# Kernel tuning notes

Measured on AMD Instinct MI355X. Metric: run time of the kernel, lower is better.

Reference implementation:

```python
import jax, jax.numpy as jnp
import numpy as np

KLD_SCALE = 10.0


def setup_inputs() -> dict:
    key = jax.random.key(0)
    k1, k2 = jax.random.split(key)
    B, C, H, W = 16, 64, 64, 64
    K = 1024
    inputs = jax.random.normal(k1, (B, C, H, W), dtype=jnp.float32)
    codebook = jax.random.normal(k2, (K, C), dtype=jnp.float32) * (1.0 / K)
    beta = jnp.float32(0.25)
    return {"inputs": inputs, "codebook": codebook, "beta": beta}


def reference(inputs, codebook, beta):
    # inputs: [B, C, H, W], codebook: [K, D] with D == C
    sg = jax.lax.stop_gradient
    x = jnp.transpose(inputs, (0, 2, 3, 1))          # [B, H, W, D]
    D = x.shape[-1]
    flat = x.reshape(-1, D)                           # [N, D]
    d = (jnp.sum(flat * flat, axis=1, keepdims=True)
         + jnp.sum(codebook * codebook, axis=1)
         - 2.0 * flat @ codebook.T)                   # [N, K]
    idx = jnp.argmin(d, axis=1)                       # [N]
    q = codebook[idx].reshape(x.shape)                # gather == one_hot @ codebook
    # training (non-EMA) loss: (beta*||q - sg(x)||^2 + ||sg(q) - x||^2) * kld_scale
    loss = beta * jnp.mean((q - sg(x)) ** 2)
    loss = (loss + jnp.mean((sg(q) - x) ** 2)) * KLD_SCALE
    # straight-through estimator
    q_st = x + sg(q - x)
    # perplexity from code usage histogram (== mean of one-hot rows)
    K = codebook.shape[0]
    counts = jnp.zeros((K,), dtype=flat.dtype).at[idx].add(1.0)
    e_mean = counts / flat.shape[0]
    perplexity = jnp.exp(-jnp.sum(e_mean * jnp.log(e_mean + 1e-10)))
    quantized = jnp.transpose(q_st, (0, 3, 1, 2))     # [B, C, H, W]
    return loss, quantized, perplexity
```

## Files before the change

### kernel.cpp

```cpp
#include <hip/hip_runtime.h>
#include <cfloat>

typedef __bf16 bf16x8 __attribute__((ext_vector_type(8)));
typedef float f32x16 __attribute__((ext_vector_type(16)));

namespace {
constexpr int kHW = 4096;
constexpr int kC = 64;
constexpr float kInvN = 1.0f / 65536.0f;


__global__ __launch_bounds__(256) void prep_kernel(
    const float* __restrict__ cb, uint4* __restrict__ frags,
    unsigned int* __restrict__ hist, float* __restrict__ lossacc) {
  const int c = blockIdx.x;
  const int t = threadIdx.x;
  const int lane = t & 63, wv = t >> 6;
  const int lo = lane & 31, hi = lane >> 5;
  const int code = c * 32 + lo;
  const int ks = wv;

  const float* row = cb + code * kC + ks * 16 + hi * 8;
  float4 v0 = *reinterpret_cast<const float4*>(row);
  float4 v1 = *reinterpret_cast<const float4*>(row + 4);
  float vv[8] = {v0.x, v0.y, v0.z, v0.w, v1.x, v1.y, v1.z, v1.w};
  bf16x8 fh, fl;
  #pragma unroll
  for (int e = 0; e < 8; ++e) {
    float v = -2.0f * vv[e];
    __bf16 h = (__bf16)v;
    fh[e] = h;
    fl[e] = (__bf16)(v - (float)h);
  }
  frags[(c * 9 + ks) * 64 + lane] = *reinterpret_cast<uint4*>(&fh);
  frags[(c * 9 + 4 + ks) * 64 + lane] = *reinterpret_cast<uint4*>(&fl);

  if (wv == 0) {
    bf16x8 fb;
    #pragma unroll
    for (int e = 0; e < 8; ++e) fb[e] = (__bf16)0.0f;
    if (hi == 0) {
      float s = 0.0f;
      #pragma unroll
      for (int d = 0; d < kC; d += 4) {
        float4 v = *reinterpret_cast<const float4*>(cb + code * kC + d);
        s = fmaf(v.x, v.x, fmaf(v.y, v.y, fmaf(v.z, v.z, fmaf(v.w, v.w, s))));
      }
      __bf16 h = (__bf16)s;
      fb[0] = h;
      fb[1] = (__bf16)(s - (float)h);
    }
    frags[(c * 9 + 8) * 64 + lane] = *reinterpret_cast<uint4*>(&fb);
  }
  if (t < 32) hist[c * 32 + t] = 0u;
  if (c == 0 && t == 0) lossacc[0] = 0.0f;
}

__global__ __launch_bounds__(256) void vq_kernel(
    const float* __restrict__ in, const bf16x8* __restrict__ frags,
    const float* __restrict__ cb, unsigned int* __restrict__ hist,
    float* __restrict__ lossacc, float* __restrict__ qout) {
  __shared__ float sVal[4][32];
  __shared__ int sIdxW[4][32];
  __shared__ int sIdx[64];
  const int t = threadIdx.x;
  const int lane = t & 63, wv = t >> 6;
  const int lo = lane & 31, hi = lane >> 5;
  const int sg2 = wv & 1, kh = wv >> 1;
  const int site = blockIdx.x * 64 + sg2 * 32 + lo;
  const int b = site >> 12, hw = site & 4095;
  const float* xp = in + b * (kC * kHW) + hw;

  bf16x8 Bh[4], Bl[4];
  #pragma unroll
  for (int ks = 0; ks < 4; ++ks) {
    #pragma unroll
    for (int e = 0; e < 8; ++e) {
      const int d = ks * 16 + hi * 8 + e;
      float v = xp[d * kHW];
      __bf16 h = (__bf16)v;
      Bh[ks][e] = h;
      Bl[ks][e] = (__bf16)(v - (float)h);
    }
  }
  bf16x8 ones;
  #pragma unroll
  for (int e = 0; e < 8; ++e) ones[e] = (__bf16)0.0f;
  if (hi == 0) { ones[0] = (__bf16)1.0f; ones[1] = (__bf16)1.0f; }
  f32x16 zero;
  #pragma unroll
  for (int r = 0; r < 16; ++r) zero[r] = 0.0f;

  float best[16];
  int bch[16];
  #pragma unroll
  for (int r = 0; r < 16; ++r) { best[r] = FLT_MAX; bch[r] = 0; }

  const bf16x8* fA = frags + lane;

  bf16x8 A0[9], A1[9];
  auto prefetch = [&](bf16x8(&F)[9], int c) {
    #pragma unroll
    for (int j = 0; j < 9; ++j) F[j] = fA[(c * 9 + j) * 64];
  };
  auto compute = [&](const bf16x8(&F)[9], int c) {
    f32x16 a = __builtin_amdgcn_mfma_f32_32x32x16_bf16(F[8], ones, zero, 0, 0, 0);
    #pragma unroll
    for (int ks = 0; ks < 4; ++ks)
      a = __builtin_amdgcn_mfma_f32_32x32x16_bf16(F[ks], Bh[ks], a, 0, 0, 0);
    #pragma unroll
    for (int ks = 0; ks < 4; ++ks)
      a = __builtin_amdgcn_mfma_f32_32x32x16_bf16(F[4 + ks], Bh[ks], a, 0, 0, 0);
    #pragma unroll
    for (int ks = 0; ks < 4; ++ks)
      a = __builtin_amdgcn_mfma_f32_32x32x16_bf16(F[ks], Bl[ks], a, 0, 0, 0);
    #pragma unroll
    for (int r = 0; r < 16; ++r) {
      bool p = a[r] < best[r];
      best[r] = p ? a[r] : best[r];
      bch[r] = p ? c : bch[r];
    }
  };

  const int c0 = kh * 16;
  prefetch(A0, c0);
  #pragma unroll 1
  for (int c = c0; c < c0 + 16; c += 2) {
    prefetch(A1, c + 1);
    compute(A0, c);
    if (c + 2 < c0 + 16) prefetch(A0, c + 2);
    compute(A1, c + 1);
  }

  float bv = best[0];
  int bidx = bch[0] * 32 + (hi << 2);
  #pragma unroll
  for (int r = 1; r < 16; ++r) {
    const int kloc = (r & 3) + 8 * (r >> 2) + (hi << 2);
    int idx = bch[r] * 32 + kloc;
    float v = best[r];
    if (v < bv || (v == bv && idx < bidx)) { bv = v; bidx = idx; }
  }
  float ov = __shfl_xor(bv, 32, 64);
  int oi = __shfl_xor(bidx, 32, 64);
  if (ov < bv || (ov == bv && oi < bidx)) { bv = ov; bidx = oi; }
  if (hi == 0) {
    sVal[wv][lo] = bv;
    sIdxW[wv][lo] = bidx;
  }
  __syncthreads();
  if (wv < 2 && hi == 0) {
    float v2 = sVal[wv + 2][lo];
    int i2 = sIdxW[wv + 2][lo];
    if (v2 < bv || (v2 == bv && i2 < bidx)) { bv = v2; bidx = i2; }
    sIdx[sg2 * 32 + lo] = bidx;
    atomicAdd(&hist[bidx], 1u);
  }
  __syncthreads();

  {
    const int s2 = t & 63;
    const int dbase = (t >> 6) * 16;
    const int gsite = blockIdx.x * 64 + s2;
    const int b2 = gsite >> 12, hw2 = gsite & 4095;
    const int code = sIdx[s2];
    const float* xr = in + b2 * (kC * kHW) + hw2;
    const float* qr = cb + code * kC + dbase;
    float* op = qout + b2 * (kC * kHW) + hw2;
    float ls = 0.0f;
    #pragma unroll
    for (int j = 0; j < 16; j += 4) {
      float4 qv = *reinterpret_cast<const float4*>(qr + j);
      float q[4] = {qv.x, qv.y, qv.z, qv.w};
      #pragma unroll
      for (int u = 0; u < 4; ++u) {
        const int d = dbase + j + u;
        float xv = xr[d * kHW];
        float diff = q[u] - xv;
        ls = fmaf(diff, diff, ls);
        op[d * kHW] = xv + diff;
      }
    }
    #pragma unroll
    for (int off = 32; off; off >>= 1) ls += __shfl_xor(ls, off, 64);
    if (lane == 0) atomicAdd(lossacc, ls);
  }
}

__global__ __launch_bounds__(1024) void finalize_kernel(
    const unsigned int* __restrict__ hist, const float* __restrict__ lossacc,
    const float* __restrict__ beta, float* __restrict__ out) {
  __shared__ float red[16];
  const int t = threadIdx.x;
  float e = (float)hist[t] * kInvN;
  float term = e * logf(e + 1e-10f);
  #pragma unroll
  for (int off = 32; off; off >>= 1) term += __shfl_xor(term, off, 64);
  if ((t & 63) == 0) red[t >> 6] = term;
  __syncthreads();
  if (t == 0) {
    float h = 0.0f;
    #pragma unroll
    for (int i = 0; i < 16; ++i) h += red[i];
    out[1 + 4194304] = expf(-h);
    out[0] = lossacc[0] * (1.0f + beta[0]) * 10.0f / 4194304.0f;
  }
}
}

extern "C" void kernel_launch(void* const* d_in, const int* in_sizes, int n_in,
                              void* d_out, int out_size, void* d_ws, size_t ws_size,
                              hipStream_t stream) {
  const float* inputs = (const float*)d_in[0];
  const float* cb = (const float*)d_in[1];
  const float* beta = (const float*)d_in[2];
  float* out = (float*)d_out;

  uint4* frags = (uint4*)d_ws;
  unsigned int* hist = (unsigned int*)((char*)d_ws + 294912);
  float* lossacc = (float*)((char*)d_ws + 294912 + 4096);

  prep_kernel<<<32, 256, 0, stream>>>(cb, (uint4*)frags, hist, lossacc);
  vq_kernel<<<1024, 256, 0, stream>>>(inputs, (const bf16x8*)d_ws, cb, hist,
                                      lossacc, out + 1);
  finalize_kernel<<<1, 1024, 0, stream>>>(hist, lossacc, beta, out);
}
```

Baseline: 139.1 us.

## Stage codebook fragments in LDS via double-buffered global_load_lds, 128 sites per block

Each block now handles 128 sites, with each wave covering 32 sites across all 32 codebook chunks instead of splitting codes between wave pairs. Codebook MFMA fragments are copied into a double-buffered LDS stage with global_load_lds and shared by all four waves, so global fragment traffic per block no longer scales with the wave count. This also removes the cross-wave argmin merge. In exchange it adds a __syncthreads per chunk, gives each wave twice the MFMA work, and halves the grid to 512 blocks, which lowers parallelism.

```diff
diff --git a/kernel.cpp b/kernel.cpp
--- a/kernel.cpp
+++ b/kernel.cpp
@@ -8,6 +8,7 @@
 constexpr int kHW = 4096;
 constexpr int kC = 64;
 constexpr float kInvN = 1.0f / 65536.0f;
+constexpr int kChunkBytes = 9216;
 
 
 __global__ __launch_bounds__(256) void prep_kernel(
@@ -57,19 +58,34 @@
 }
 
 __global__ __launch_bounds__(256) void vq_kernel(
-    const float* __restrict__ in, const bf16x8* __restrict__ frags,
+    const float* __restrict__ in, const char* __restrict__ fragsB,
     const float* __restrict__ cb, unsigned int* __restrict__ hist,
     float* __restrict__ lossacc, float* __restrict__ qout) {
-  __shared__ float sVal[4][32];
-  __shared__ int sIdxW[4][32];
-  __shared__ int sIdx[64];
+  __shared__ __align__(16) char sStage[2 * kChunkBytes];
+  __shared__ int sIdx[128];
   const int t = threadIdx.x;
   const int lane = t & 63, wv = t >> 6;
   const int lo = lane & 31, hi = lane >> 5;
-  const int sg2 = wv & 1, kh = wv >> 1;
-  const int site = blockIdx.x * 64 + sg2 * 32 + lo;
+  const int site = blockIdx.x * 128 + wv * 32 + lo;
   const int b = site >> 12, hw = site & 4095;
   const float* xp = in + b * (kC * kHW) + hw;
+
+  auto stage = [&](int buf, int c) {
+    const char* g = fragsB + (size_t)c * kChunkBytes;
+    char* l0 = sStage + buf * kChunkBytes;
+    __builtin_amdgcn_global_load_lds(
+        (const uint32_t*)(g + wv * 1024 + lane * 16),
+        (uint32_t*)(l0 + wv * 1024), 16, 0, 0);
+    __builtin_amdgcn_global_load_lds(
+        (const uint32_t*)(g + 4096 + wv * 1024 + lane * 16),
+        (uint32_t*)(l0 + 4096 + wv * 1024), 16, 0, 0);
+    if (wv == 0)
+      __builtin_amdgcn_global_load_lds(
+          (const uint32_t*)(g + 8192 + lane * 16),
+          (uint32_t*)(l0 + 8192), 16, 0, 0);
+  };
+
+  stage(0, 0);
 
   bf16x8 Bh[4], Bl[4];
   #pragma unroll
@@ -96,15 +112,22 @@
   #pragma unroll
   for (int r = 0; r < 16; ++r) { best[r] = FLT_MAX; bch[r] = 0; }
 
-  const bf16x8* fA = frags + lane;
-
-  bf16x8 A0[9], A1[9];
-  auto prefetch = [&](bf16x8(&F)[9], int c) {
-    #pragma unroll
-    for (int j = 0; j < 9; ++j) F[j] = fA[(c * 9 + j) * 64];
-  };
-  auto compute = [&](const bf16x8(&F)[9], int c) {
-    f32x16 a = __builtin_amdgcn_mfma_f32_32x32x16_bf16(F[8], ones, zero, 0, 0, 0);
+  asm volatile("s_waitcnt vmcnt(0)" ::: "memory");
+  __syncthreads();
+
+  int buf = 0;
+  #pragma unroll 1
+  for (int c = 0; c < 32; ++c) {
+    if (c + 1 < 32) stage(buf ^ 1, c + 1);
+
+    const char* lb = sStage + buf * kChunkBytes;
+    bf16x8 F8 = *reinterpret_cast<const bf16x8*>(lb + 8 * 1024 + lane * 16);
+    bf16x8 F[8];
+    #pragma unroll
+    for (int j = 0; j < 8; ++j)
+      F[j] = *reinterpret_cast<const bf16x8*>(lb + j * 1024 + lane * 16);
+
+    f32x16 a = __builtin_amdgcn_mfma_f32_32x32x16_bf16(F8, ones, zero, 0, 0, 0);
     #pragma unroll
     for (int ks = 0; ks < 4; ++ks)
       a = __builtin_amdgcn_mfma_f32_32x32x16_bf16(F[ks], Bh[ks], a, 0, 0, 0);
@@ -120,16 +143,9 @@
       best[r] = p ? a[r] : best[r];
       bch[r] = p ? c : bch[r];
     }
-  };
-
-  const int c0 = kh * 16;
-  prefetch(A0, c0);
-  #pragma unroll 1
-  for (int c = c0; c < c0 + 16; c += 2) {
-    prefetch(A1, c + 1);
-    compute(A0, c);
-    if (c + 2 < c0 + 16) prefetch(A0, c + 2);
-    compute(A1, c + 1);
+
+    __syncthreads();
+    buf ^= 1;
   }
 
   float bv = best[0];
@@ -145,23 +161,15 @@
   int oi = __shfl_xor(bidx, 32, 64);
   if (ov < bv || (ov == bv && oi < bidx)) { bv = ov; bidx = oi; }
   if (hi == 0) {
-    sVal[wv][lo] = bv;
-    sIdxW[wv][lo] = bidx;
+    sIdx[wv * 32 + lo] = bidx;
+    atomicAdd(&hist[bidx], 1u);
   }
   __syncthreads();
-  if (wv < 2 && hi == 0) {
-    float v2 = sVal[wv + 2][lo];
-    int i2 = sIdxW[wv + 2][lo];
-    if (v2 < bv || (v2 == bv && i2 < bidx)) { bv = v2; bidx = i2; }
-    sIdx[sg2 * 32 + lo] = bidx;
-    atomicAdd(&hist[bidx], 1u);
-  }
-  __syncthreads();
 
   {
-    const int s2 = t & 63;
-    const int dbase = (t >> 6) * 16;
-    const int gsite = blockIdx.x * 64 + s2;
+    const int s2 = t & 127;
+    const int dbase = (t >> 7) << 5;
+    const int gsite = blockIdx.x * 128 + s2;
     const int b2 = gsite >> 12, hw2 = gsite & 4095;
     const int code = sIdx[s2];
     const float* xr = in + b2 * (kC * kHW) + hw2;
@@ -169,7 +177,7 @@
     float* op = qout + b2 * (kC * kHW) + hw2;
     float ls = 0.0f;
     #pragma unroll
-    for (int j = 0; j < 16; j += 4) {
+    for (int j = 0; j < 32; j += 4) {
       float4 qv = *reinterpret_cast<const float4*>(qr + j);
       float q[4] = {qv.x, qv.y, qv.z, qv.w};
       #pragma unroll
@@ -220,8 +228,8 @@
   unsigned int* hist = (unsigned int*)((char*)d_ws + 294912);
   float* lossacc = (float*)((char*)d_ws + 294912 + 4096);
 
-  prep_kernel<<<32, 256, 0, stream>>>(cb, (uint4*)frags, hist, lossacc);
-  vq_kernel<<<1024, 256, 0, stream>>>(inputs, (const bf16x8*)d_ws, cb, hist,
-                                      lossacc, out + 1);
+  prep_kernel<<<32, 256, 0, stream>>>(cb, frags, hist, lossacc);
+  vq_kernel<<<512, 256, 0, stream>>>(inputs, (const char*)d_ws, cb, hist,
+                                     lossacc, out + 1);
   finalize_kernel<<<1, 1024, 0, stream>>>(hist, lossacc, beta, out);
 }
```

New measurement: 138.3 us. About the same (-0.6%).

## Split VQ epilogue into separate kernel with vectorized per-site loads and stores

Applied to the files above, without the earlier changes.

Splits the fused argmin-plus-writeback kernel in two. The argmin kernel now writes each site's code index to workspace. A new epilogue kernel handles 4 contiguous sites per thread with float4 input loads, gathers codebook rows, writes the straight-through output, and reduces the loss per block before one atomic. This aims to free the argmin kernel from the strided scalar epilogue and widen memory accesses, at the cost of an extra launch, re-reading the input, and a round trip for the indices.

```diff
diff --git a/kernel.cpp b/kernel.cpp
--- a/kernel.cpp
+++ b/kernel.cpp
@@ -56,13 +56,11 @@
   if (c == 0 && t == 0) lossacc[0] = 0.0f;
 }
 
-__global__ __launch_bounds__(256) void vq_kernel(
+__global__ __launch_bounds__(256) void vq_argmin_kernel(
     const float* __restrict__ in, const bf16x8* __restrict__ frags,
-    const float* __restrict__ cb, unsigned int* __restrict__ hist,
-    float* __restrict__ lossacc, float* __restrict__ qout) {
+    unsigned int* __restrict__ hist, unsigned int* __restrict__ idxOut) {
   __shared__ float sVal[4][32];
   __shared__ int sIdxW[4][32];
-  __shared__ int sIdx[64];
   const int t = threadIdx.x;
   const int lane = t & 63, wv = t >> 6;
   const int lo = lane & 31, hi = lane >> 5;
@@ -153,37 +151,53 @@
     float v2 = sVal[wv + 2][lo];
     int i2 = sIdxW[wv + 2][lo];
     if (v2 < bv || (v2 == bv && i2 < bidx)) { bv = v2; bidx = i2; }
-    sIdx[sg2 * 32 + lo] = bidx;
+    idxOut[site] = (unsigned int)bidx;
     atomicAdd(&hist[bidx], 1u);
   }
+}
+
+__global__ __launch_bounds__(256) void epilogue_kernel(
+    const float* __restrict__ in, const float* __restrict__ cb,
+    const unsigned int* __restrict__ idx, float* __restrict__ lossacc,
+    float* __restrict__ qout) {
+  __shared__ float sRed[4];
+  const int t = threadIdx.x;
+  const int sg = t & 63, dg = t >> 6;
+  const int siteBase = blockIdx.x * 256 + sg * 4;
+  const int b = siteBase >> 12, hw = siteBase & 4095;
+  const float* xb = in + b * (kC * kHW) + hw;
+  float* ob = qout + b * (kC * kHW) + hw;
+  uint4 cc = *reinterpret_cast<const uint4*>(idx + siteBase);
+  const float* q0 = cb + cc.x * kC;
+  const float* q1 = cb + cc.y * kC;
+  const float* q2 = cb + cc.z * kC;
+  const float* q3 = cb + cc.w * kC;
+  float ls = 0.0f;
+  #pragma unroll
+  for (int j = 0; j < 16; ++j) {
+    const int d = dg * 16 + j;
+    float4 xv = *reinterpret_cast<const float4*>(xb + d * kHW);
+    float d0 = q0[d] - xv.x;
+    float d1 = q1[d] - xv.y;
+    float d2 = q2[d] - xv.z;
+    float d3 = q3[d] - xv.w;
+    ls = fmaf(d0, d0, ls);
+    ls = fmaf(d1, d1, ls);
+    ls = fmaf(d2, d2, ls);
+    ls = fmaf(d3, d3, ls);
+    float* o = ob + d * kHW;
+    o[0] = xv.x + d0;
+    o[1] = xv.y + d1;
+    o[2] = xv.z + d2;
+    o[3] = xv.w + d3;
+  }
+  #pragma unroll
+  for (int off = 32; off; off >>= 1) ls += __shfl_xor(ls, off, 64);
+  if ((t & 63) == 0) sRed[t >> 6] = ls;
   __syncthreads();
-
-  {
-    const int s2 = t & 63;
-    const int dbase = (t >> 6) * 16;
-    const int gsite = blockIdx.x * 64 + s2;
-    const int b2 = gsite >> 12, hw2 = gsite & 4095;
-    const int code = sIdx[s2];
-    const float* xr = in + b2 * (kC * kHW) + hw2;
-    const float* qr = cb + code * kC + dbase;
-    float* op = qout + b2 * (kC * kHW) + hw2;
-    float ls = 0.0f;
-    #pragma unroll
-    for (int j = 0; j < 16; j += 4) {
-      float4 qv = *reinterpret_cast<const float4*>(qr + j);
-      float q[4] = {qv.x, qv.y, qv.z, qv.w};
-      #pragma unroll
-      for (int u = 0; u < 4; ++u) {
-        const int d = dbase + j + u;
-        float xv = xr[d * kHW];
-        float diff = q[u] - xv;
-        ls = fmaf(diff, diff, ls);
-        op[d * kHW] = xv + diff;
-      }
-    }
-    #pragma unroll
-    for (int off = 32; off; off >>= 1) ls += __shfl_xor(ls, off, 64);
-    if (lane == 0) atomicAdd(lossacc, ls);
+  if (t == 0) {
+    float s = (sRed[0] + sRed[1]) + (sRed[2] + sRed[3]);
+    atomicAdd(lossacc, s);
   }
 }
 
@@ -218,10 +232,12 @@
 
   uint4* frags = (uint4*)d_ws;
   unsigned int* hist = (unsigned int*)((char*)d_ws + 294912);
-  float* lossacc = (float*)((char*)d_ws + 294912 + 4096);
-
-  prep_kernel<<<32, 256, 0, stream>>>(cb, (uint4*)frags, hist, lossacc);
-  vq_kernel<<<1024, 256, 0, stream>>>(inputs, (const bf16x8*)d_ws, cb, hist,
-                                      lossacc, out + 1);
+  float* lossacc = (float*)((char*)d_ws + 299008);
+  unsigned int* idx = (unsigned int*)((char*)d_ws + 299024);
+
+  prep_kernel<<<32, 256, 0, stream>>>(cb, frags, hist, lossacc);
+  vq_argmin_kernel<<<1024, 256, 0, stream>>>(inputs, (const bf16x8*)frags,
+                                             hist, idx);
+  epilogue_kernel<<<256, 256, 0, stream>>>(inputs, cb, idx, lossacc, out + 1);
   finalize_kernel<<<1, 1024, 0, stream>>>(hist, lossacc, beta, out);
 }
```

Result: faster. 121.2 us (-12.9%).
